# Kernel optimization log

Measured on AMD Instinct MI355X. Metric: run time of the kernel, lower is better.

The kernel has to match this reference:

```python
import jax, jax.numpy as jnp
import numpy as np

B, S, H = 2, 2048, 2048
NH = 16
HD = H // NH  # 128


def setup_inputs() -> dict:
    key = jax.random.key(0)
    ks = jax.random.split(key, 10)
    std = 0.02
    hidden_states = jax.random.normal(ks[0], (B, S, H), dtype=jnp.float32)
    # causal additive mask, broadcastable to [B, NH, S, S]
    causal = jnp.tril(jnp.ones((S, S), dtype=jnp.float32))
    attention_mask = jnp.where(causal == 1, 0.0, -1e9)[None, None, :, :] * jnp.ones((B, 1, 1, 1), jnp.float32)
    Wq = jax.random.normal(ks[1], (H, H), jnp.float32) * std
    Wk = jax.random.normal(ks[2], (H, H), jnp.float32) * std
    Wv = jax.random.normal(ks[3], (H, H), jnp.float32) * std
    Wo = jax.random.normal(ks[4], (H, H), jnp.float32) * std
    bq = jnp.zeros((H,), jnp.float32)
    bk = jnp.zeros((H,), jnp.float32)
    bv = jnp.zeros((H,), jnp.float32)
    bo = jnp.zeros((H,), jnp.float32)
    return {"hidden_states": hidden_states, "attention_mask": attention_mask,
            "Wq": Wq, "bq": bq, "Wk": Wk, "bk": bk, "Wv": Wv, "bv": bv, "Wo": Wo, "bo": bo}


def reference(hidden_states, attention_mask, Wq, bq, Wk, bk, Wv, bv, Wo, bo):
    b, s, _ = hidden_states.shape
    q = (hidden_states @ Wq + bq).reshape(b, s, NH, HD)
    k = (hidden_states @ Wk + bk).reshape(b, s, NH, HD)
    v = (hidden_states @ Wv + bv).reshape(b, s, NH, HD)
    # [b, h, s_q, s_k]
    scores = jnp.einsum('bqhd,bkhd->bhqk', q, k) / jnp.sqrt(jnp.float32(HD))
    scores = scores + attention_mask
    probs = jax.nn.softmax(scores, axis=-1)
    out = jnp.einsum('bhqk,bkhd->bqhd', probs, v).reshape(b, s, H)
    return out @ Wo + bo
```

## Files before the change

kernel.cpp:

```cpp
#include <hip/hip_runtime.h>
#include <hip/hip_bf16.h>
#include <stdint.h>

#define SEQ 2048
#define HID 2048
#define NHEAD 16
#define HDIM 128

typedef __attribute__((ext_vector_type(8))) short short8;
typedef __attribute__((ext_vector_type(4))) float f32x4;

__device__ __forceinline__ short f2bf(float f) {
  union { float f; unsigned u; } x; x.f = f;
  unsigned r = (x.u + 0x7FFFu + ((x.u >> 16) & 1u)) >> 16;
  return (short)r;
}

__device__ __forceinline__ void async_ld16(const void* g, void* l) {
  __builtin_amdgcn_global_load_lds(
      (__attribute__((address_space(1))) void*)g,
      (__attribute__((address_space(3))) void*)l, 16, 0, 0);
}

__global__ __launch_bounds__(256) void k_convert(const float* __restrict__ X,
                                                 short* __restrict__ Xb) {
  int i = blockIdx.x * 256 + threadIdx.x;
  float4 v = ((const float4*)X)[i];
  short4 o;
  o.x = f2bf(v.x); o.y = f2bf(v.y); o.z = f2bf(v.z); o.w = f2bf(v.w);
  ((short4*)Xb)[i] = o;
}

__global__ __launch_bounds__(256) void k_transpose(const float* __restrict__ W0,
                                                   const float* __restrict__ W1,
                                                   const float* __restrict__ W2,
                                                   const float* __restrict__ W3,
                                                   short* __restrict__ Wt) {
  __shared__ float t[32][33];
  int z = blockIdx.z;
  const float* W = (z == 0) ? W0 : (z == 1) ? W1 : (z == 2) ? W2 : W3;
  short* o = Wt + (size_t)z * HID * HID;
  int k0 = blockIdx.x * 32, n0 = blockIdx.y * 32;
  int tx = threadIdx.x, ty = threadIdx.y;
  for (int i = 0; i < 4; ++i) {
    int r = ty + i * 8;
    t[r][tx] = W[(size_t)(k0 + r) * HID + n0 + tx];
  }
  __syncthreads();
  for (int i = 0; i < 4; ++i) {
    int r = ty + i * 8;
    o[(size_t)(n0 + r) * HID + k0 + tx] = f2bf(t[tx][r]);
  }
}

__global__ __launch_bounds__(256, 3) void k_gemm_qkv(const short* __restrict__ A,
                                                     const short* __restrict__ Bt,
                                                     const float* __restrict__ bqp,
                                                     const float* __restrict__ bkp,
                                                     const float* __restrict__ bvp,
                                                     short* __restrict__ Qb,
                                                     short* __restrict__ Kb,
                                                     short* __restrict__ VtG) {
  __shared__ short smem[128 * 136];
  short* As = smem;
  short* Bs = smem + 128 * 64;
  const int tid = threadIdx.x;
  const int wave = tid >> 6, lane = tid & 63;
  const int col = lane & 15, quad = lane >> 4;
  const int wm = wave >> 1, wn = wave & 1;
  const int m0 = blockIdx.y * 128;
  const int n0g = blockIdx.x * 128;
  const int j = n0g >> 11;
  const int n0 = n0g & 2047;
  const int K = HID;
  const float* bias = (j == 0) ? bqp : (j == 1) ? bkp : bvp;

  const int rS = (lane >> 3), cS = lane & 7;
  f32x4 acc[4][4];
  for (int i = 0; i < 4; ++i)
    for (int jj = 0; jj < 4; ++jj)
      acc[i][jj] = (f32x4){0.f, 0.f, 0.f, 0.f};

  for (int k0 = 0; k0 < K; k0 += 64) {
    __syncthreads();
    for (int i = 0; i < 4; ++i) {
      int rowb = wave * 8 + i * 32;
      int row = rowb + rS;
      int src = cS ^ (row & 7);
      async_ld16(A + (size_t)(m0 + row) * K + k0 + src * 8,
                 (char*)As + (size_t)rowb * 128);
      async_ld16(Bt + (size_t)(n0g + row) * K + k0 + src * 8,
                 (char*)Bs + (size_t)rowb * 128);
    }
    __syncthreads();
    for (int h = 0; h < 2; ++h) {
      short8 af[4], bf[4];
      for (int mi = 0; mi < 4; ++mi)
        af[mi] = *(const short8*)(As + (wm * 64 + mi * 16 + col) * 64 +
                                  ((h * 4 + quad) ^ (col & 7)) * 8);
      for (int ni = 0; ni < 4; ++ni)
        bf[ni] = *(const short8*)(Bs + (wn * 64 + ni * 16 + col) * 64 +
                                  ((h * 4 + quad) ^ (col & 7)) * 8);
      for (int mi = 0; mi < 4; ++mi)
        for (int ni = 0; ni < 4; ++ni)
          acc[mi][ni] =
              __builtin_amdgcn_mfma_f32_16x16x32_bf16(af[mi], bf[ni], acc[mi][ni], 0, 0, 0);
    }
  }

  __syncthreads();
  short* T = smem;
  if (j == 2) {
    for (int ni = 0; ni < 4; ++ni) {
      int n = wn * 64 + ni * 16 + col;
      float bv = bias[n0 + n];
      for (int mi = 0; mi < 4; ++mi)
        for (int r = 0; r < 4; ++r) {
          int m = wm * 64 + mi * 16 + quad * 4 + r;
          T[n * 136 + m] = f2bf(acc[mi][ni][r] + bv);
        }
    }
    __syncthreads();
    int h = n0 >> 7;
    int b = m0 >> 11, s0l = m0 & 2047;
    int rr = tid >> 1, halfc = tid & 1;
    short* o = VtG + ((size_t)(b * NHEAD + h) * HDIM + rr) * SEQ + s0l;
    for (int i = 0; i < 8; ++i) {
      int chunk = halfc * 8 + i;
      short8 v = *(const short8*)(T + rr * 136 + chunk * 8);
      *(short8*)(o + chunk * 8) = v;
    }
    return;
  }

  for (int ni = 0; ni < 4; ++ni) {
    int n = wn * 64 + ni * 16 + col;
    float bv = bias[n0 + n];
    for (int mi = 0; mi < 4; ++mi)
      for (int r = 0; r < 4; ++r) {
        int m = wm * 64 + mi * 16 + quad * 4 + r;
        T[m * 136 + n] = f2bf(acc[mi][ni][r] + bv);
      }
  }
  __syncthreads();
  short* out = (j == 0) ? Qb : Kb;
  int h = n0 >> 7;
  for (int i = 0; i < 8; ++i) {
    int c = i * 256 + tid;
    int m = c >> 4, ch = c & 15;
    int mm = m0 + m;
    int b = mm >> 11, s = mm & 2047;
    short8 v = *(const short8*)(T + m * 136 + ch * 8);
    *(short8*)(out + ((size_t)(b * NHEAD + h) * SEQ + s) * HDIM + ch * 8) = v;
  }
}

__global__ __launch_bounds__(256, 3) void k_gemm_o(const short* __restrict__ A,
                                                   const short* __restrict__ Bt,
                                                   const float* __restrict__ bias,
                                                   float* __restrict__ out) {
  __shared__ short As[128 * 64];
  __shared__ short Bs[128 * 64];
  const int tid = threadIdx.x;
  const int wave = tid >> 6, lane = tid & 63;
  const int col = lane & 15, quad = lane >> 4;
  const int wm = wave >> 1, wn = wave & 1;
  const int m0 = blockIdx.y * 128, n0 = blockIdx.x * 128;
  const int K = HID;
  const int rS = (lane >> 3), cS = lane & 7;

  f32x4 acc[4][4];
  for (int i = 0; i < 4; ++i)
    for (int jj = 0; jj < 4; ++jj)
      acc[i][jj] = (f32x4){0.f, 0.f, 0.f, 0.f};

  for (int k0 = 0; k0 < K; k0 += 64) {
    __syncthreads();
    for (int i = 0; i < 4; ++i) {
      int rowb = wave * 8 + i * 32;
      int row = rowb + rS;
      int src = cS ^ (row & 7);
      async_ld16(A + (size_t)(m0 + row) * K + k0 + src * 8,
                 (char*)As + (size_t)rowb * 128);
      async_ld16(Bt + (size_t)(n0 + row) * K + k0 + src * 8,
                 (char*)Bs + (size_t)rowb * 128);
    }
    __syncthreads();
    for (int h = 0; h < 2; ++h) {
      short8 af[4], bf[4];
      for (int mi = 0; mi < 4; ++mi)
        af[mi] = *(const short8*)(As + (wm * 64 + mi * 16 + col) * 64 +
                                  ((h * 4 + quad) ^ (col & 7)) * 8);
      for (int ni = 0; ni < 4; ++ni)
        bf[ni] = *(const short8*)(Bs + (wn * 64 + ni * 16 + col) * 64 +
                                  ((h * 4 + quad) ^ (col & 7)) * 8);
      for (int mi = 0; mi < 4; ++mi)
        for (int ni = 0; ni < 4; ++ni)
          acc[mi][ni] =
              __builtin_amdgcn_mfma_f32_16x16x32_bf16(af[mi], bf[ni], acc[mi][ni], 0, 0, 0);
    }
  }

  for (int ni = 0; ni < 4; ++ni) {
    int n = n0 + wn * 64 + ni * 16 + col;
    float bv = bias[n];
    for (int mi = 0; mi < 4; ++mi)
      for (int r = 0; r < 4; ++r) {
        int m = m0 + wm * 64 + mi * 16 + quad * 4 + r;
        out[(size_t)m * HID + n] = acc[mi][ni][r] + bv;
      }
  }
}

__global__ __launch_bounds__(1024) void k_attn(const short* __restrict__ Qb,
                                               const short* __restrict__ Kb,
                                               const short* __restrict__ VtG,
                                               short* __restrict__ AO) {
  __shared__ short Ks[2][64 * 128];
  __shared__ short Vt[2][128 * 64];
  __shared__ short Pb[16 * 16 * 72];

  const int bx = blockIdx.x;
  const int p = bx & 7;
  const int h = (bx >> 3) & 15;
  const int b = bx >> 7;
  const int tid = threadIdx.x;
  const int wave = tid >> 6, lane = tid & 63;
  const int col = lane & 15, quad = lane >> 4;

  const bool hiw = wave < 8;
  const int wslot = wave & 7;
  const int qb = hiw ? (15 - p) : p;
  const int q0 = qb * 128 + wslot * 16;
  const int nt_w = 2 * qb + 2;
  const int nt = 2 * (15 - p) + 2;

  const size_t ho = (size_t)(b * NHEAD + h) * SEQ * HDIM;
  const short* Qh = Qb + ho;
  const short* Kh = Kb + ho;
  const short* Vh = VtG + ho;

  const float scale = 0.08838834764831845f;
  short8 ones;
  for (int i = 0; i < 8; ++i) ones[i] = (short)0x3F80;

  const int rowK = tid >> 4, c16 = tid & 15;
  const int srcK = c16 ^ (rowK & 7);
  const int rowV = tid >> 3, c8 = tid & 7;
  const int srcV = c8 ^ (rowV & 7);
  short* Pw = Pb + wave * 16 * 72;

  short8 qf[4];
  for (int f = 0; f < 4; ++f)
    qf[f] = *(const short8*)(Qh + (size_t)(q0 + col) * HDIM + f * 32 + quad * 8);

  f32x4 o[8], osum;
  for (int t = 0; t < 8; ++t) o[t] = (f32x4){0.f, 0.f, 0.f, 0.f};
  osum = (f32x4){0.f, 0.f, 0.f, 0.f};

  async_ld16(Kh + (size_t)rowK * HDIM + srcK * 8, (char*)Ks[0] + tid * 16);
  async_ld16(Vh + (size_t)rowV * SEQ + srcV * 8, (char*)Vt[0] + tid * 16);

  for (int kb = 0; kb < nt; ++kb) {
    __syncthreads();
    const int cur = kb & 1;
    if (kb + 1 < nt) {
      async_ld16(Kh + (size_t)((kb + 1) * 64 + rowK) * HDIM + srcK * 8,
                 (char*)Ks[cur ^ 1] + tid * 16);
      async_ld16(Vh + (size_t)rowV * SEQ + (kb + 1) * 64 + srcV * 8,
                 (char*)Vt[cur ^ 1] + tid * 16);
    }
    if (kb >= nt_w) continue;

    const short* KsC = Ks[cur];
    const short* VtC = Vt[cur];

    f32x4 s[4];
    for (int nf = 0; nf < 4; ++nf) s[nf] = (f32x4){0.f, 0.f, 0.f, 0.f};
    for (int f = 0; f < 4; ++f)
      for (int nf = 0; nf < 4; ++nf) {
        short8 kf = *(const short8*)(KsC + (nf * 16 + col) * 128 +
                                     (((f * 4 + quad) ^ (col & 7)) * 8));
        s[nf] = __builtin_amdgcn_mfma_f32_16x16x32_bf16(qf[f], kf, s[nf], 0, 0, 0);
      }

    const bool diag = (kb >= 2 * qb);
    for (int nf = 0; nf < 4; ++nf)
      for (int r = 0; r < 4; ++r) {
        float e = __expf(s[nf][r] * scale - 8.0f);
        if (diag) {
          int key = kb * 64 + nf * 16 + col;
          int q = q0 + quad * 4 + r;
          if (key > q) e = 0.f;
        }
        Pw[(quad * 4 + r) * 72 + nf * 16 + col] = f2bf(e);
      }

    for (int kk = 0; kk < 2; ++kk) {
      short8 pa = *(const short8*)(Pw + col * 72 + kk * 32 + quad * 8);
      osum = __builtin_amdgcn_mfma_f32_16x16x32_bf16(pa, ones, osum, 0, 0, 0);
      for (int t = 0; t < 8; ++t) {
        short8 vf = *(const short8*)(VtC + (t * 16 + col) * 64 +
                                     (((kk * 4 + quad) ^ (col & 7)) * 8));
        o[t] = __builtin_amdgcn_mfma_f32_16x16x32_bf16(pa, vf, o[t], 0, 0, 0);
      }
    }
  }

  for (int r = 0; r < 4; ++r) {
    float inv = 1.f / osum[r];
    int q = q0 + quad * 4 + r;
    for (int t = 0; t < 8; ++t)
      AO[((size_t)(b * SEQ + q)) * HID + h * HDIM + 16 * t + col] = f2bf(o[t][r] * inv);
  }
}

extern "C" void kernel_launch(void* const* d_in, const int* in_sizes, int n_in,
                              void* d_out, int out_size, void* d_ws, size_t ws_size,
                              hipStream_t stream) {
  const float* X  = (const float*)d_in[0];
  const float* Wq = (const float*)d_in[2];
  const float* bq = (const float*)d_in[3];
  const float* Wk = (const float*)d_in[4];
  const float* bk = (const float*)d_in[5];
  const float* Wv = (const float*)d_in[6];
  const float* bv = (const float*)d_in[7];
  const float* Wo = (const float*)d_in[8];
  const float* bo = (const float*)d_in[9];

  char* ws = (char*)d_ws;
  short* Xb  = (short*)(ws);
  short* Wt  = (short*)(ws + (16ull << 20));
  short* Qb  = (short*)(ws + (48ull << 20));
  short* Kb  = (short*)(ws + (64ull << 20));
  short* VtG = (short*)(ws + (80ull << 20));
  short* AO  = (short*)(ws + (96ull << 20));

  short* Wto = Wt + (size_t)3 * HID * HID;

  k_convert<<<8192, 256, 0, stream>>>(X, Xb);
  k_transpose<<<dim3(64, 64, 4), dim3(32, 8), 0, stream>>>(Wq, Wk, Wv, Wo, Wt);

  k_gemm_qkv<<<dim3(48, 32), 256, 0, stream>>>(Xb, Wt, bq, bk, bv, Qb, Kb, VtG);

  k_attn<<<2 * NHEAD * 8, 1024, 0, stream>>>(Qb, Kb, VtG, AO);

  k_gemm_o<<<dim3(16, 32), 256, 0, stream>>>(AO, Wto, bo, (float*)d_out);
}
```

Baseline: 381.6 us.

## Rewrite QKV GEMM with 256x256 tiles, double-buffered async prefetch and block swizzle

```diff
diff --git a/kernel.cpp b/kernel.cpp
--- a/kernel.cpp
+++ b/kernel.cpp
@@ -53,7 +53,7 @@
   }
 }
 
-__global__ __launch_bounds__(256, 3) void k_gemm_qkv(const short* __restrict__ A,
+__global__ __launch_bounds__(512, 2) void k_gemm_qkv(const short* __restrict__ A,
                                                      const short* __restrict__ Bt,
                                                      const float* __restrict__ bqp,
                                                      const float* __restrict__ bkp,
@@ -61,21 +61,174 @@
                                                      short* __restrict__ Qb,
                                                      short* __restrict__ Kb,
                                                      short* __restrict__ VtG) {
-  __shared__ short smem[128 * 136];
-  short* As = smem;
-  short* Bs = smem + 128 * 64;
+  __shared__ short sm[2][2][256 * 64];
+  const int tid = threadIdx.x;
+  const int wave = tid >> 6, lane = tid & 63;
+  const int col = lane & 15, quad = lane >> 4;
+  const int wm = wave >> 2, wn = wave & 3;
+
+  const int bid = blockIdx.x;
+  const int swz = (bid & 7) * 48 + (bid >> 3);
+  const int bx = swz % 24, by = swz / 24;
+  const int m0 = by * 256;
+  const int n0g = bx * 256;
+  const int j = n0g >> 11;
+  const int n0 = n0g & 2047;
+  const float* bias = (j == 0) ? bqp : (j == 1) ? bkp : bvp;
+
+  const size_t lgoff = (size_t)(lane >> 3) * HID + (size_t)(((lane & 7) ^ (lane >> 3)) * 8);
+  const int wrow = wave * 16;
+  auto stage = [&](const short* g, short* lds) {
+    async_ld16(g + lgoff, (char*)lds + wrow * 128);
+    async_ld16(g + 8 * HID + lgoff, (char*)lds + wrow * 128 + 1024);
+  };
+  auto Ag = [&](int t, int h) { return A + (size_t)(m0 + h * 128 + wrow) * HID + t * 64; };
+  auto Bg = [&](int t, int h) { return Bt + (size_t)(n0g + h * 128 + wrow) * HID + t * 64; };
+
+  f32x4 acc[8][4];
+#pragma unroll
+  for (int i = 0; i < 8; ++i)
+#pragma unroll
+    for (int jj = 0; jj < 4; ++jj) acc[i][jj] = (f32x4){0.f, 0.f, 0.f, 0.f};
+
+  stage(Bg(0, 0), &sm[0][1][0]);
+  stage(Bg(0, 1), &sm[0][1][8192]);
+  stage(Ag(0, 0), &sm[0][0][0]);
+  stage(Ag(0, 1), &sm[0][0][8192]);
+  stage(Bg(1, 0), &sm[1][1][0]);
+  stage(Bg(1, 1), &sm[1][1][8192]);
+  stage(Ag(1, 0), &sm[1][0][0]);
+  asm volatile("s_waitcnt vmcnt(6)" ::: "memory");
+  __builtin_amdgcn_s_barrier();
+
+  const int T = HID / 64;
+  short8 bfr[4][2];
+  for (int t = 0; t < T; ++t) {
+    const int cur = t & 1;
+    const short* Ab = &sm[cur][0][0];
+    const short* Bb = &sm[cur][1][0];
+#pragma unroll
+    for (int p = 0; p < 4; ++p) {
+      if (p == 0) {
+#pragma unroll
+        for (int ni = 0; ni < 4; ++ni)
+#pragma unroll
+          for (int ks = 0; ks < 2; ++ks)
+            bfr[ni][ks] = *(const short8*)(Bb + (wn * 64 + ni * 16 + col) * 64 +
+                                           ((ks * 4 + quad) ^ (col & 7)) * 8);
+      }
+      short8 afr[2][2];
+#pragma unroll
+      for (int d = 0; d < 2; ++d)
+#pragma unroll
+        for (int ks = 0; ks < 2; ++ks)
+          afr[d][ks] = *(const short8*)(Ab + (wm * 128 + (p * 2 + d) * 16 + col) * 64 +
+                                        ((ks * 4 + quad) ^ (col & 7)) * 8);
+      if (p == 0 && t + 1 < T) stage(Ag(t + 1, 1), &sm[cur ^ 1][0][8192]);
+      if (p == 1 && t + 2 < T) stage(Bg(t + 2, 0), &sm[cur][1][0]);
+      if (p == 2 && t + 2 < T) stage(Bg(t + 2, 1), &sm[cur][1][8192]);
+      if (p == 3 && t + 2 < T) stage(Ag(t + 2, 0), &sm[cur][0][0]);
+      __builtin_amdgcn_s_barrier();
+      asm volatile("s_waitcnt lgkmcnt(0)" ::: "memory");
+      __builtin_amdgcn_sched_barrier(0);
+      __builtin_amdgcn_s_setprio(1);
+#pragma unroll
+      for (int ks = 0; ks < 2; ++ks)
+#pragma unroll
+        for (int d = 0; d < 2; ++d)
+#pragma unroll
+          for (int ni = 0; ni < 4; ++ni)
+            acc[p * 2 + d][ni] = __builtin_amdgcn_mfma_f32_16x16x32_bf16(
+                afr[d][ks], bfr[ni][ks], acc[p * 2 + d][ni], 0, 0, 0);
+      __builtin_amdgcn_s_setprio(0);
+      if (p == 3) {
+        if (t + 2 < T) {
+          asm volatile("s_waitcnt vmcnt(6)" ::: "memory");
+        } else if (t + 1 < T) {
+          asm volatile("s_waitcnt vmcnt(0)" ::: "memory");
+        }
+      }
+      __builtin_amdgcn_s_barrier();
+    }
+  }
+
+  short* Tb = &sm[0][0][0];
+  if (j == 2) {
+    const int b = m0 >> 11;
+#pragma unroll
+    for (int H = 0; H < 2; ++H) {
+      if (wm == H) {
+#pragma unroll
+        for (int ni = 0; ni < 4; ++ni) {
+          const int n = wn * 64 + ni * 16 + col;
+          const float bv = bias[n0 + n];
+#pragma unroll
+          for (int mi = 0; mi < 8; ++mi) {
+            short4 v4;
+            v4.x = f2bf(acc[mi][ni][0] + bv);
+            v4.y = f2bf(acc[mi][ni][1] + bv);
+            v4.z = f2bf(acc[mi][ni][2] + bv);
+            v4.w = f2bf(acc[mi][ni][3] + bv);
+            *(short4*)(Tb + n * 136 + mi * 16 + quad * 4) = v4;
+          }
+        }
+      }
+      __syncthreads();
+      for (int it = 0; it < 8; ++it) {
+        int c = it * 512 + tid;
+        int n = c >> 4, ch = c & 15;
+        int ng = n0 + n;
+        short8 v = *(const short8*)(Tb + n * 136 + ch * 8);
+        *(short8*)(VtG + ((size_t)(b * NHEAD + (ng >> 7)) * HDIM + (ng & 127)) * SEQ +
+                   (m0 & 2047) + H * 128 + ch * 8) = v;
+      }
+      __syncthreads();
+    }
+    return;
+  }
+  short* out = (j == 0) ? Qb : Kb;
+#pragma unroll
+  for (int H = 0; H < 2; ++H) {
+    if (wm == H) {
+#pragma unroll
+      for (int ni = 0; ni < 4; ++ni) {
+        const int n = wn * 64 + ni * 16 + col;
+        const float bv = bias[n0 + n];
+#pragma unroll
+        for (int mi = 0; mi < 8; ++mi)
+#pragma unroll
+          for (int r = 0; r < 4; ++r)
+            Tb[(mi * 16 + quad * 4 + r) * 264 + n] = f2bf(acc[mi][ni][r] + bv);
+      }
+    }
+    __syncthreads();
+    for (int it = 0; it < 8; ++it) {
+      int c = it * 512 + tid;
+      int m = c >> 5, ch = c & 31;
+      int mm = m0 + H * 128 + m;
+      int ng = n0 + ch * 8;
+      short8 v = *(const short8*)(Tb + m * 264 + ch * 8);
+      *(short8*)(out + ((size_t)((mm >> 11) * NHEAD + (ng >> 7)) * SEQ + (mm & 2047)) * HDIM +
+                 (ng & 127)) = v;
+    }
+    __syncthreads();
+  }
+}
+
+__global__ __launch_bounds__(256, 3) void k_gemm_o(const short* __restrict__ A,
+                                                   const short* __restrict__ Bt,
+                                                   const float* __restrict__ bias,
+                                                   float* __restrict__ out) {
+  __shared__ short As[128 * 64];
+  __shared__ short Bs[128 * 64];
   const int tid = threadIdx.x;
   const int wave = tid >> 6, lane = tid & 63;
   const int col = lane & 15, quad = lane >> 4;
   const int wm = wave >> 1, wn = wave & 1;
-  const int m0 = blockIdx.y * 128;
-  const int n0g = blockIdx.x * 128;
-  const int j = n0g >> 11;
-  const int n0 = n0g & 2047;
+  const int m0 = blockIdx.y * 128, n0 = blockIdx.x * 128;
   const int K = HID;
-  const float* bias = (j == 0) ? bqp : (j == 1) ? bkp : bvp;
-
   const int rS = (lane >> 3), cS = lane & 7;
+
   f32x4 acc[4][4];
   for (int i = 0; i < 4; ++i)
     for (int jj = 0; jj < 4; ++jj)
@@ -89,7 +242,7 @@
       int src = cS ^ (row & 7);
       async_ld16(A + (size_t)(m0 + row) * K + k0 + src * 8,
                  (char*)As + (size_t)rowb * 128);
-      async_ld16(Bt + (size_t)(n0g + row) * K + k0 + src * 8,
+      async_ld16(Bt + (size_t)(n0 + row) * K + k0 + src * 8,
                  (char*)Bs + (size_t)rowb * 128);
     }
     __syncthreads();
@@ -108,99 +261,6 @@
     }
   }
 
-  __syncthreads();
-  short* T = smem;
-  if (j == 2) {
-    for (int ni = 0; ni < 4; ++ni) {
-      int n = wn * 64 + ni * 16 + col;
-      float bv = bias[n0 + n];
-      for (int mi = 0; mi < 4; ++mi)
-        for (int r = 0; r < 4; ++r) {
-          int m = wm * 64 + mi * 16 + quad * 4 + r;
-          T[n * 136 + m] = f2bf(acc[mi][ni][r] + bv);
-        }
-    }
-    __syncthreads();
-    int h = n0 >> 7;
-    int b = m0 >> 11, s0l = m0 & 2047;
-    int rr = tid >> 1, halfc = tid & 1;
-    short* o = VtG + ((size_t)(b * NHEAD + h) * HDIM + rr) * SEQ + s0l;
-    for (int i = 0; i < 8; ++i) {
-      int chunk = halfc * 8 + i;
-      short8 v = *(const short8*)(T + rr * 136 + chunk * 8);
-      *(short8*)(o + chunk * 8) = v;
-    }
-    return;
-  }
-
-  for (int ni = 0; ni < 4; ++ni) {
-    int n = wn * 64 + ni * 16 + col;
-    float bv = bias[n0 + n];
-    for (int mi = 0; mi < 4; ++mi)
-      for (int r = 0; r < 4; ++r) {
-        int m = wm * 64 + mi * 16 + quad * 4 + r;
-        T[m * 136 + n] = f2bf(acc[mi][ni][r] + bv);
-      }
-  }
-  __syncthreads();
-  short* out = (j == 0) ? Qb : Kb;
-  int h = n0 >> 7;
-  for (int i = 0; i < 8; ++i) {
-    int c = i * 256 + tid;
-    int m = c >> 4, ch = c & 15;
-    int mm = m0 + m;
-    int b = mm >> 11, s = mm & 2047;
-    short8 v = *(const short8*)(T + m * 136 + ch * 8);
-    *(short8*)(out + ((size_t)(b * NHEAD + h) * SEQ + s) * HDIM + ch * 8) = v;
-  }
-}
-
-__global__ __launch_bounds__(256, 3) void k_gemm_o(const short* __restrict__ A,
-                                                   const short* __restrict__ Bt,
-                                                   const float* __restrict__ bias,
-                                                   float* __restrict__ out) {
-  __shared__ short As[128 * 64];
-  __shared__ short Bs[128 * 64];
-  const int tid = threadIdx.x;
-  const int wave = tid >> 6, lane = tid & 63;
-  const int col = lane & 15, quad = lane >> 4;
-  const int wm = wave >> 1, wn = wave & 1;
-  const int m0 = blockIdx.y * 128, n0 = blockIdx.x * 128;
-  const int K = HID;
-  const int rS = (lane >> 3), cS = lane & 7;
-
-  f32x4 acc[4][4];
-  for (int i = 0; i < 4; ++i)
-    for (int jj = 0; jj < 4; ++jj)
-      acc[i][jj] = (f32x4){0.f, 0.f, 0.f, 0.f};
-
-  for (int k0 = 0; k0 < K; k0 += 64) {
-    __syncthreads();
-    for (int i = 0; i < 4; ++i) {
-      int rowb = wave * 8 + i * 32;
-      int row = rowb + rS;
-      int src = cS ^ (row & 7);
-      async_ld16(A + (size_t)(m0 + row) * K + k0 + src * 8,
-                 (char*)As + (size_t)rowb * 128);
-      async_ld16(Bt + (size_t)(n0 + row) * K + k0 + src * 8,
-                 (char*)Bs + (size_t)rowb * 128);
-    }
-    __syncthreads();
-    for (int h = 0; h < 2; ++h) {
-      short8 af[4], bf[4];
-      for (int mi = 0; mi < 4; ++mi)
-        af[mi] = *(const short8*)(As + (wm * 64 + mi * 16 + col) * 64 +
-                                  ((h * 4 + quad) ^ (col & 7)) * 8);
-      for (int ni = 0; ni < 4; ++ni)
-        bf[ni] = *(const short8*)(Bs + (wn * 64 + ni * 16 + col) * 64 +
-                                  ((h * 4 + quad) ^ (col & 7)) * 8);
-      for (int mi = 0; mi < 4; ++mi)
-        for (int ni = 0; ni < 4; ++ni)
-          acc[mi][ni] =
-              __builtin_amdgcn_mfma_f32_16x16x32_bf16(af[mi], bf[ni], acc[mi][ni], 0, 0, 0);
-    }
-  }
-
   for (int ni = 0; ni < 4; ++ni) {
     int n = n0 + wn * 64 + ni * 16 + col;
     float bv = bias[n];
@@ -341,7 +401,7 @@
   k_convert<<<8192, 256, 0, stream>>>(X, Xb);
   k_transpose<<<dim3(64, 64, 4), dim3(32, 8), 0, stream>>>(Wq, Wk, Wv, Wo, Wt);
 
-  k_gemm_qkv<<<dim3(48, 32), 256, 0, stream>>>(Xb, Wt, bq, bk, bv, Qb, Kb, VtG);
+  k_gemm_qkv<<<384, 512, 0, stream>>>(Xb, Wt, bq, bk, bv, Qb, Kb, VtG);
 
   k_attn<<<2 * NHEAD * 8, 1024, 0, stream>>>(Qb, Kb, VtG, AO);
 
```

After: 391.9 us. 1.03x slower.

## Use 32x32 MFMA tiles in attention with 512-thread blocks; swizzle GEMM tiles

Applied to the files above, without the earlier changes.

```diff
diff --git a/kernel.cpp b/kernel.cpp
--- a/kernel.cpp
+++ b/kernel.cpp
@@ -9,6 +9,7 @@
 
 typedef __attribute__((ext_vector_type(8))) short short8;
 typedef __attribute__((ext_vector_type(4))) float f32x4;
+typedef __attribute__((ext_vector_type(16))) float f32x16;
 
 __device__ __forceinline__ short f2bf(float f) {
   union { float f; unsigned u; } x; x.f = f;
@@ -68,8 +69,10 @@
   const int wave = tid >> 6, lane = tid & 63;
   const int col = lane & 15, quad = lane >> 4;
   const int wm = wave >> 1, wn = wave & 1;
-  const int m0 = blockIdx.y * 128;
-  const int n0g = blockIdx.x * 128;
+  const int flat = blockIdx.y * 48 + blockIdx.x;
+  const int swz = (flat & 7) * 192 + (flat >> 3);
+  const int m0 = (swz / 48) * 128;
+  const int n0g = (swz % 48) * 128;
   const int j = n0g >> 11;
   const int n0 = n0g & 2047;
   const int K = HID;
@@ -165,7 +168,9 @@
   const int wave = tid >> 6, lane = tid & 63;
   const int col = lane & 15, quad = lane >> 4;
   const int wm = wave >> 1, wn = wave & 1;
-  const int m0 = blockIdx.y * 128, n0 = blockIdx.x * 128;
+  const int flat = blockIdx.y * 16 + blockIdx.x;
+  const int swz = (flat & 7) * 64 + (flat >> 3);
+  const int m0 = (swz / 16) * 128, n0 = (swz % 16) * 128;
   const int K = HID;
   const int rS = (lane >> 3), cS = lane & 7;
 
@@ -212,13 +217,13 @@
   }
 }
 
-__global__ __launch_bounds__(1024) void k_attn(const short* __restrict__ Qb,
-                                               const short* __restrict__ Kb,
-                                               const short* __restrict__ VtG,
-                                               short* __restrict__ AO) {
+__global__ __launch_bounds__(512, 2) void k_attn(const short* __restrict__ Qb,
+                                                 const short* __restrict__ Kb,
+                                                 const short* __restrict__ VtG,
+                                                 short* __restrict__ AO) {
   __shared__ short Ks[2][64 * 128];
   __shared__ short Vt[2][128 * 64];
-  __shared__ short Pb[16 * 16 * 72];
+  __shared__ short Pb[8 * 32 * 72];
 
   const int bx = blockIdx.x;
   const int p = bx & 7;
@@ -226,13 +231,13 @@
   const int b = bx >> 7;
   const int tid = threadIdx.x;
   const int wave = tid >> 6, lane = tid & 63;
-  const int col = lane & 15, quad = lane >> 4;
-
-  const bool hiw = wave < 8;
-  const int wslot = wave & 7;
+  const int l31 = lane & 31, hi = lane >> 5;
+
+  const bool hiw = wave < 4;
+  const int wslot = wave & 3;
   const int qb = hiw ? (15 - p) : p;
-  const int q0 = qb * 128 + wslot * 16;
-  const int nt_w = 2 * qb + 2;
+  const int q0 = qb * 128 + wslot * 32;
+  const int nt_w = 2 * qb + 1 + (wslot >> 1);
   const int nt = 2 * (15 - p) + 2;
 
   const size_t ho = (size_t)(b * NHEAD + h) * SEQ * HDIM;
@@ -244,74 +249,92 @@
   short8 ones;
   for (int i = 0; i < 8; ++i) ones[i] = (short)0x3F80;
 
-  const int rowK = tid >> 4, c16 = tid & 15;
-  const int srcK = c16 ^ (rowK & 7);
-  const int rowV = tid >> 3, c8 = tid & 7;
-  const int srcV = c8 ^ (rowV & 7);
-  short* Pw = Pb + wave * 16 * 72;
-
-  short8 qf[4];
-  for (int f = 0; f < 4; ++f)
-    qf[f] = *(const short8*)(Qh + (size_t)(q0 + col) * HDIM + f * 32 + quad * 8);
-
-  f32x4 o[8], osum;
-  for (int t = 0; t < 8; ++t) o[t] = (f32x4){0.f, 0.f, 0.f, 0.f};
-  osum = (f32x4){0.f, 0.f, 0.f, 0.f};
-
-  async_ld16(Kh + (size_t)rowK * HDIM + srcK * 8, (char*)Ks[0] + tid * 16);
-  async_ld16(Vh + (size_t)rowV * SEQ + srcV * 8, (char*)Vt[0] + tid * 16);
+  short* Pw = Pb + wave * 32 * 72;
+
+  short8 qf[8];
+#pragma unroll
+  for (int ds = 0; ds < 8; ++ds)
+    qf[ds] = *(const short8*)(Qh + (size_t)(q0 + l31) * HDIM + ds * 16 + hi * 8);
+
+  f32x16 o0, o1, o2, o3, osum;
+#pragma unroll
+  for (int r = 0; r < 16; ++r) { o0[r] = 0.f; o1[r] = 0.f; o2[r] = 0.f; o3[r] = 0.f; osum[r] = 0.f; }
+
+#define STAGE_KV(kb_, buf_)                                                      \
+  {                                                                              \
+    _Pragma("unroll") for (int half = 0; half < 2; ++half) {                     \
+      int g = half * 512 + tid;                                                  \
+      int rK = g >> 4, sK = g & 15;                                              \
+      async_ld16(Kh + (size_t)((kb_)*64 + rK) * HDIM + (sK ^ (rK & 7)) * 8,      \
+                 (char*)Ks[buf_] + (size_t)g * 16);                              \
+      int rV = g >> 3, sV = g & 7;                                               \
+      async_ld16(Vh + (size_t)rV * SEQ + (kb_)*64 + (sV ^ (rV & 7)) * 8,         \
+                 (char*)Vt[buf_] + (size_t)g * 16);                              \
+    }                                                                            \
+  }
+
+  STAGE_KV(0, 0);
 
   for (int kb = 0; kb < nt; ++kb) {
     __syncthreads();
     const int cur = kb & 1;
-    if (kb + 1 < nt) {
-      async_ld16(Kh + (size_t)((kb + 1) * 64 + rowK) * HDIM + srcK * 8,
-                 (char*)Ks[cur ^ 1] + tid * 16);
-      async_ld16(Vh + (size_t)rowV * SEQ + (kb + 1) * 64 + srcV * 8,
-                 (char*)Vt[cur ^ 1] + tid * 16);
-    }
+    if (kb + 1 < nt) STAGE_KV(kb + 1, cur ^ 1);
     if (kb >= nt_w) continue;
 
     const short* KsC = Ks[cur];
     const short* VtC = Vt[cur];
 
-    f32x4 s[4];
-    for (int nf = 0; nf < 4; ++nf) s[nf] = (f32x4){0.f, 0.f, 0.f, 0.f};
-    for (int f = 0; f < 4; ++f)
-      for (int nf = 0; nf < 4; ++nf) {
-        short8 kf = *(const short8*)(KsC + (nf * 16 + col) * 128 +
-                                     (((f * 4 + quad) ^ (col & 7)) * 8));
-        s[nf] = __builtin_amdgcn_mfma_f32_16x16x32_bf16(qf[f], kf, s[nf], 0, 0, 0);
+    f32x16 s0, s1;
+#pragma unroll
+    for (int r = 0; r < 16; ++r) { s0[r] = 0.f; s1[r] = 0.f; }
+#pragma unroll
+    for (int ds = 0; ds < 8; ++ds) {
+      short8 k0 = *(const short8*)(KsC + l31 * 128 + ((ds * 2 + hi) ^ (l31 & 7)) * 8);
+      s0 = __builtin_amdgcn_mfma_f32_32x32x16_bf16(qf[ds], k0, s0, 0, 0, 0);
+      short8 k1 = *(const short8*)(KsC + (32 + l31) * 128 + ((ds * 2 + hi) ^ (l31 & 7)) * 8);
+      s1 = __builtin_amdgcn_mfma_f32_32x32x16_bf16(qf[ds], k1, s1, 0, 0, 0);
+    }
+
+    const bool diag = (kb >= 2 * qb);
+#pragma unroll
+    for (int r = 0; r < 16; ++r) {
+      int row = (r & 3) + 8 * (r >> 2) + 4 * hi;
+      float e0 = __expf(s0[r] * scale - 8.0f);
+      float e1 = __expf(s1[r] * scale - 8.0f);
+      if (diag) {
+        int q = q0 + row;
+        if (kb * 64 + l31 > q) e0 = 0.f;
+        if (kb * 64 + 32 + l31 > q) e1 = 0.f;
       }
-
-    const bool diag = (kb >= 2 * qb);
-    for (int nf = 0; nf < 4; ++nf)
-      for (int r = 0; r < 4; ++r) {
-        float e = __expf(s[nf][r] * scale - 8.0f);
-        if (diag) {
-          int key = kb * 64 + nf * 16 + col;
-          int q = q0 + quad * 4 + r;
-          if (key > q) e = 0.f;
-        }
-        Pw[(quad * 4 + r) * 72 + nf * 16 + col] = f2bf(e);
-      }
-
-    for (int kk = 0; kk < 2; ++kk) {
-      short8 pa = *(const short8*)(Pw + col * 72 + kk * 32 + quad * 8);
-      osum = __builtin_amdgcn_mfma_f32_16x16x32_bf16(pa, ones, osum, 0, 0, 0);
-      for (int t = 0; t < 8; ++t) {
-        short8 vf = *(const short8*)(VtC + (t * 16 + col) * 64 +
-                                     (((kk * 4 + quad) ^ (col & 7)) * 8));
-        o[t] = __builtin_amdgcn_mfma_f32_16x16x32_bf16(pa, vf, o[t], 0, 0, 0);
-      }
-    }
-  }
-
-  for (int r = 0; r < 4; ++r) {
+      Pw[row * 72 + l31] = f2bf(e0);
+      Pw[row * 72 + 32 + l31] = f2bf(e1);
+    }
+
+#pragma unroll
+    for (int ks = 0; ks < 4; ++ks) {
+      short8 pa = *(const short8*)(Pw + l31 * 72 + ks * 16 + hi * 8);
+      osum = __builtin_amdgcn_mfma_f32_32x32x16_bf16(pa, ones, osum, 0, 0, 0);
+      short8 v0 = *(const short8*)(VtC + l31 * 64 + ((ks * 2 + hi) ^ (l31 & 7)) * 8);
+      o0 = __builtin_amdgcn_mfma_f32_32x32x16_bf16(pa, v0, o0, 0, 0, 0);
+      short8 v1 = *(const short8*)(VtC + (32 + l31) * 64 + ((ks * 2 + hi) ^ (l31 & 7)) * 8);
+      o1 = __builtin_amdgcn_mfma_f32_32x32x16_bf16(pa, v1, o1, 0, 0, 0);
+      short8 v2 = *(const short8*)(VtC + (64 + l31) * 64 + ((ks * 2 + hi) ^ (l31 & 7)) * 8);
+      o2 = __builtin_amdgcn_mfma_f32_32x32x16_bf16(pa, v2, o2, 0, 0, 0);
+      short8 v3 = *(const short8*)(VtC + (96 + l31) * 64 + ((ks * 2 + hi) ^ (l31 & 7)) * 8);
+      o3 = __builtin_amdgcn_mfma_f32_32x32x16_bf16(pa, v3, o3, 0, 0, 0);
+    }
+  }
+
+#pragma unroll
+  for (int r = 0; r < 16; ++r) {
+    int row = (r & 3) + 8 * (r >> 2) + 4 * hi;
+    int q = q0 + row;
     float inv = 1.f / osum[r];
-    int q = q0 + quad * 4 + r;
-    for (int t = 0; t < 8; ++t)
-      AO[((size_t)(b * SEQ + q)) * HID + h * HDIM + 16 * t + col] = f2bf(o[t][r] * inv);
+    short* dst = AO + ((size_t)(b * SEQ + q)) * HID + h * HDIM + l31;
+    dst[0] = f2bf(o0[r] * inv);
+    dst[32] = f2bf(o1[r] * inv);
+    dst[64] = f2bf(o2[r] * inv);
+    dst[96] = f2bf(o3[r] * inv);
   }
 }
 
@@ -343,7 +366,7 @@
 
   k_gemm_qkv<<<dim3(48, 32), 256, 0, stream>>>(Xb, Wt, bq, bk, bv, Qb, Kb, VtG);
 
-  k_attn<<<2 * NHEAD * 8, 1024, 0, stream>>>(Qb, Kb, VtG, AO);
+  k_attn<<<2 * NHEAD * 8, 512, 0, stream>>>(Qb, Kb, VtG, AO);
 
   k_gemm_o<<<dim3(16, 32), 256, 0, stream>>>(AO, Wto, bo, (float*)d_out);
 }
```

Result: slower. 409.5 us (+7.3%).
